# Kernel optimization log

Hardware: AMD Instinct MI355X
Metric: run time of the kernel (lower is better)

Reference implementation:

```python
import jax, jax.numpy as jnp
import numpy as np

NUM_EMBEDDINGS = 1024
EMBEDDING_DIM = 64


def setup_inputs() -> dict:
    key = jax.random.key(0)
    k1, k2 = jax.random.split(key)
    x = jax.random.normal(k1, (32, 64, 32, 32), dtype=jnp.float32)
    # embeddings initialized uniform(-1/K, 1/K) as in the torch module
    codebook = jax.random.uniform(
        k2, (NUM_EMBEDDINGS, EMBEDDING_DIM), dtype=jnp.float32,
        minval=-1.0 / NUM_EMBEDDINGS, maxval=1.0 / NUM_EMBEDDINGS)
    return {"x": x, "codebook": codebook}


def reference(x, codebook):
    # x: [B, D, H, W] -> [B, H, W, D]
    xp = jnp.transpose(x, (0, 2, 3, 1))
    B, H, W, D = xp.shape
    K = codebook.shape[0]
    xf = xp.reshape(-1, D)  # [N, D]
    # squared L2 distances via expansion (argmin identical to torch.norm argmin)
    x2 = jnp.sum(xf * xf, axis=1, keepdims=True)          # [N, 1]
    c2 = jnp.sum(codebook * codebook, axis=1)             # [K]
    d2 = x2 - 2.0 * (xf @ codebook.T) + c2[None, :]       # [N, K]
    idx = jnp.argmin(d2, axis=1)                          # [N]
    encodings = jax.nn.one_hot(idx, K, dtype=jnp.float32)  # [N, K]
    quantized = codebook[idx]                             # [N, D] == encodings @ codebook
    quantized = quantized.reshape(B, H, W, D).transpose(0, 3, 1, 2)
    return encodings, quantized
```

## Files before the change

kernel.cpp:

```cpp
#include <hip/hip_runtime.h>

#define N_PIX   32768
#define DIM     64
#define K_CODES 1024
#define NCHUNK  8
#define CHUNK   (K_CODES / NCHUNK)


__global__ __launch_bounds__(256) void c2_kernel(const float* __restrict__ cb,
                                                 float* __restrict__ c2) {
    int k = blockIdx.x * 256 + threadIdx.x;
    if (k >= K_CODES) return;
    const float* row = cb + k * DIM;
    float a0 = 0.f, a1 = 0.f, a2 = 0.f, a3 = 0.f;
#pragma unroll
    for (int d = 0; d < DIM; d += 4) {
        a0 = fmaf(row[d + 0], row[d + 0], a0);
        a1 = fmaf(row[d + 1], row[d + 1], a1);
        a2 = fmaf(row[d + 2], row[d + 2], a2);
        a3 = fmaf(row[d + 3], row[d + 3], a3);
    }
    c2[k] = (a0 + a1) + (a2 + a3);
}

__global__ __launch_bounds__(256, 4) void argmin_lds(const float* __restrict__ x,
                                                     const float* __restrict__ cb,
                                                     const float* __restrict__ c2,
                                                     float2* __restrict__ part) {
    __shared__ alignas(16) float lds_cb[CHUNK][DIM];
    __shared__ float lds_c2[CHUNK];

    int blk    = blockIdx.x;
    int pixblk = blk >> 3;
    int chunk  = blk & 7;
    int t  = threadIdx.x;
    int k0 = chunk * CHUNK;

    {
        const float4* cb4  = reinterpret_cast<const float4*>(cb) + (size_t)k0 * (DIM / 4);
        float4*       lds4 = reinterpret_cast<float4*>(&lds_cb[0][0]);
#pragma unroll
        for (int i = 0; i < (CHUNK * DIM / 4) / 256; ++i)
            lds4[t + i * 256] = cb4[t + i * 256];
        if (t < CHUNK) lds_c2[t] = c2[k0 + t];
    }

    int p  = pixblk * 256 + t;
    int bb = p >> 10;
    int hw = p & 1023;

    const float* xbase = x + (size_t)bb * (DIM * 1024) + hw;
    float xv[DIM];
#pragma unroll
    for (int d = 0; d < DIM; ++d) xv[d] = xbase[(size_t)d << 10];

    float s0 = 0.f, s1 = 0.f, s2 = 0.f, s3 = 0.f;
#pragma unroll
    for (int d = 0; d < DIM; d += 4) {
        s0 = fmaf(xv[d + 0], xv[d + 0], s0);
        s1 = fmaf(xv[d + 1], xv[d + 1], s1);
        s2 = fmaf(xv[d + 2], xv[d + 2], s2);
        s3 = fmaf(xv[d + 3], xv[d + 3], s3);
    }
    float x2 = (s0 + s1) + (s2 + s3);

    __syncthreads();

    float best = 1e30f;
    int   bidx = 0;
#pragma unroll 2
    for (int kk = 0; kk < CHUNK; ++kk) {
        const float* crow = &lds_cb[kk][0];
        float c2k = lds_c2[kk];
        float a0 = 0.f, a1 = 0.f, a2 = 0.f, a3 = 0.f;
#pragma unroll
        for (int d = 0; d < DIM; d += 4) {
            float4 w = *reinterpret_cast<const float4*>(crow + d);
            a0 = fmaf(xv[d + 0], w.x, a0);
            a1 = fmaf(xv[d + 1], w.y, a1);
            a2 = fmaf(xv[d + 2], w.z, a2);
            a3 = fmaf(xv[d + 3], w.w, a3);
        }
        float dot = (a0 + a1) + (a2 + a3);
        float u    = x2 - 2.0f * dot;
        float dist = u + c2k;
        int   k    = k0 + kk;
        if (dist < best) { best = dist; bidx = k; }
    }
    float2 r;
    r.x = best;
    r.y = __int_as_float(bidx);
    part[(size_t)chunk * N_PIX + p] = r;
}

__global__ __launch_bounds__(128) void reduce_quant(const float* __restrict__ cb,
                                                    const float2* __restrict__ part,
                                                    int* __restrict__ idx,
                                                    float* __restrict__ quant) {
    int n = blockIdx.x * 128 + threadIdx.x;
    float best = 1e30f;
    int   bi = 0;
#pragma unroll
    for (int c = 0; c < NCHUNK; ++c) {
        float2 r = part[(size_t)c * N_PIX + n];
        if (r.x < best) { best = r.x; bi = __float_as_int(r.y); }
    }
    idx[n] = bi;

    int bb = n >> 10;
    int hw = n & 1023;
    const float4* crow = reinterpret_cast<const float4*>(cb + (size_t)bi * DIM);
    float* qb = quant + (size_t)bb * (DIM * 1024) + hw;
#pragma unroll
    for (int dq = 0; dq < 16; ++dq) {
        float4 cv = crow[dq];
        qb[(size_t)(dq * 4 + 0) << 10] = cv.x;
        qb[(size_t)(dq * 4 + 1) << 10] = cv.y;
        qb[(size_t)(dq * 4 + 2) << 10] = cv.z;
        qb[(size_t)(dq * 4 + 3) << 10] = cv.w;
    }
}

__global__ __launch_bounds__(256) void enc_write(const int* __restrict__ idx,
                                                 float* __restrict__ enc) {
    const int TOT = (N_PIX / 4) * K_CODES;
    int tid = blockIdx.x * 256 + threadIdx.x;
    float4* enc4 = reinterpret_cast<float4*>(enc);
    for (int e = tid; e < TOT; e += 2048 * 256) {
        int n  = e >> 8;
        int j0 = (e & 255) << 2;
        int ir = idx[n];
        float4 v;
        v.x = (ir == j0 + 0) ? 1.0f : 0.0f;
        v.y = (ir == j0 + 1) ? 1.0f : 0.0f;
        v.z = (ir == j0 + 2) ? 1.0f : 0.0f;
        v.w = (ir == j0 + 3) ? 1.0f : 0.0f;
        enc4[e] = v;
    }
}

extern "C" void kernel_launch(void* const* d_in, const int* in_sizes, int n_in,
                              void* d_out, int out_size, void* d_ws, size_t ws_size,
                              hipStream_t stream) {
    const float* x  = (const float*)d_in[0];
    const float* cb = (const float*)d_in[1];

    float*  c2   = (float*)d_ws;
    float2* part = (float2*)((char*)d_ws + 4096);
    int*    idx  = (int*)((char*)d_ws + 4096 + (size_t)NCHUNK * N_PIX * 8);

    float* enc   = (float*)d_out;
    float* quant = (float*)d_out + (size_t)N_PIX * K_CODES;

    c2_kernel<<<K_CODES / 256, 256, 0, stream>>>(cb, c2);
    argmin_lds<<<(N_PIX / 256) * NCHUNK, 256, 0, stream>>>(x, cb, c2, part);
    reduce_quant<<<N_PIX / 128, 128, 0, stream>>>(cb, part, idx, quant);
    enc_write<<<2048, 256, 0, stream>>>(idx, enc);
}
```

Baseline: 255.0 us.

## Replace per-pixel argmin with register-tiled GEMM-style kernel fused with quantize

Replaces the per-thread dot-product argmin, which held 64 x values per thread and split the codebook into 8 chunks with a separate partial reduction, with a 128-pixel by 1024-code register-tiled kernel. Each thread computes an 8x8 outer-product tile from LDS-staged transposed x and codebook slices, prefetching the next codebook chunk into registers while computing. The argmin is reduced in-block via shuffles and LDS, and the quantized gather/write is fused in, removing the partial buffer and the reduce kernel. It raises register and LDS pressure and adds index tie-breaking that the previous code did not have.

```diff
diff --git a/kernel.cpp b/kernel.cpp
--- a/kernel.cpp
+++ b/kernel.cpp
@@ -1,10 +1,12 @@
 #include <hip/hip_runtime.h>
 
-#define N_PIX   32768
-#define DIM     64
-#define K_CODES 1024
-#define NCHUNK  8
-#define CHUNK   (K_CODES / NCHUNK)
+#define N_PIX    32768
+#define DIM      64
+#define K_CODES  1024
+#define NCHUNK   4
+#define CHUNK    256
+#define BPIX     128
+#define CS_STR   260
 
 
 __global__ __launch_bounds__(256) void c2_kernel(const float* __restrict__ cb,
@@ -23,101 +25,169 @@
     c2[k] = (a0 + a1) + (a2 + a3);
 }
 
-__global__ __launch_bounds__(256, 4) void argmin_lds(const float* __restrict__ x,
-                                                     const float* __restrict__ cb,
-                                                     const float* __restrict__ c2,
-                                                     float2* __restrict__ part) {
-    __shared__ alignas(16) float lds_cb[CHUNK][DIM];
-    __shared__ float lds_c2[CHUNK];
-
-    int blk    = blockIdx.x;
-    int pixblk = blk >> 3;
-    int chunk  = blk & 7;
-    int t  = threadIdx.x;
-    int k0 = chunk * CHUNK;
-
-    {
-        const float4* cb4  = reinterpret_cast<const float4*>(cb) + (size_t)k0 * (DIM / 4);
-        float4*       lds4 = reinterpret_cast<float4*>(&lds_cb[0][0]);
-#pragma unroll
-        for (int i = 0; i < (CHUNK * DIM / 4) / 256; ++i)
-            lds4[t + i * 256] = cb4[t + i * 256];
-        if (t < CHUNK) lds_c2[t] = c2[k0 + t];
-    }
-
-    int p  = pixblk * 256 + t;
-    int bb = p >> 10;
-    int hw = p & 1023;
-
-    const float* xbase = x + (size_t)bb * (DIM * 1024) + hw;
-    float xv[DIM];
-#pragma unroll
-    for (int d = 0; d < DIM; ++d) xv[d] = xbase[(size_t)d << 10];
-
-    float s0 = 0.f, s1 = 0.f, s2 = 0.f, s3 = 0.f;
-#pragma unroll
-    for (int d = 0; d < DIM; d += 4) {
-        s0 = fmaf(xv[d + 0], xv[d + 0], s0);
-        s1 = fmaf(xv[d + 1], xv[d + 1], s1);
-        s2 = fmaf(xv[d + 2], xv[d + 2], s2);
-        s3 = fmaf(xv[d + 3], xv[d + 3], s3);
-    }
-    float x2 = (s0 + s1) + (s2 + s3);
-
+__global__ __launch_bounds__(512, 2) void argmin_tile(const float* __restrict__ x,
+                                                      const float* __restrict__ cb,
+                                                      const float* __restrict__ c2,
+                                                      int* __restrict__ idx,
+                                                      float* __restrict__ quant) {
+    __shared__ alignas(16) float xs[DIM * BPIX];
+    __shared__ alignas(16) float cs[DIM * CS_STR];
+    __shared__ float  xn[BPIX];
+    __shared__ float2 red[4][BPIX];
+
+    const int t      = threadIdx.x;
+    const int blk    = blockIdx.x;
+    const int p_base = blk * BPIX;
+    const int bb     = p_base >> 10;
+    const int hw0    = p_base & 1023;
+
+    const float4* x4  = reinterpret_cast<const float4*>(x);
+    const float4* cb4 = reinterpret_cast<const float4*>(cb);
+
+#pragma unroll
+    for (int i = 0; i < 4; ++i) {
+        int fidx = i * 512 + t;
+        int d = fidx >> 5, p4 = fidx & 31;
+        float4 v = x4[(size_t)bb * 16384 + (size_t)d * 256 + (hw0 >> 2) + p4];
+        *reinterpret_cast<float4*>(&xs[d * BPIX + p4 * 4]) = v;
+    }
     __syncthreads();
 
-    float best = 1e30f;
-    int   bidx = 0;
-#pragma unroll 2
-    for (int kk = 0; kk < CHUNK; ++kk) {
-        const float* crow = &lds_cb[kk][0];
-        float c2k = lds_c2[kk];
-        float a0 = 0.f, a1 = 0.f, a2 = 0.f, a3 = 0.f;
+    if (t < BPIX) {
+        float s0 = 0.f, s1 = 0.f, s2 = 0.f, s3 = 0.f;
 #pragma unroll
         for (int d = 0; d < DIM; d += 4) {
-            float4 w = *reinterpret_cast<const float4*>(crow + d);
-            a0 = fmaf(xv[d + 0], w.x, a0);
-            a1 = fmaf(xv[d + 1], w.y, a1);
-            a2 = fmaf(xv[d + 2], w.z, a2);
-            a3 = fmaf(xv[d + 3], w.w, a3);
-        }
-        float dot = (a0 + a1) + (a2 + a3);
-        float u    = x2 - 2.0f * dot;
-        float dist = u + c2k;
-        int   k    = k0 + kk;
-        if (dist < best) { best = dist; bidx = k; }
-    }
-    float2 r;
-    r.x = best;
-    r.y = __int_as_float(bidx);
-    part[(size_t)chunk * N_PIX + p] = r;
-}
-
-__global__ __launch_bounds__(128) void reduce_quant(const float* __restrict__ cb,
-                                                    const float2* __restrict__ part,
-                                                    int* __restrict__ idx,
-                                                    float* __restrict__ quant) {
-    int n = blockIdx.x * 128 + threadIdx.x;
-    float best = 1e30f;
-    int   bi = 0;
-#pragma unroll
+            float v0 = xs[(d + 0) * BPIX + t];
+            float v1 = xs[(d + 1) * BPIX + t];
+            float v2 = xs[(d + 2) * BPIX + t];
+            float v3 = xs[(d + 3) * BPIX + t];
+            s0 = fmaf(v0, v0, s0);
+            s1 = fmaf(v1, v1, s1);
+            s2 = fmaf(v2, v2, s2);
+            s3 = fmaf(v3, v3, s3);
+        }
+        xn[t] = (s0 + s1) + (s2 + s3);
+    }
+
+    const int lane = t & 63, w = t >> 6;
+    const int wy = lane >> 3, wx = lane & 7;
+    const int wr = w >> 2,    wc = w & 3;
+    const int pl0 = wr * 64 + wy * 8;
+    const int kl0 = wc * 64 + wx * 8;
+
+    float bv[8]; int bk[8]; float xnr[8];
+#pragma unroll
+    for (int i = 0; i < 8; ++i) { bv[i] = 1e30f; bk[i] = 0; }
+
+    float4 creg[8];
+#pragma unroll
+    for (int i = 0; i < 8; ++i) {
+        int fidx = i * 512 + t; int k = fidx & 255, dq = fidx >> 8;
+        creg[i] = cb4[(size_t)k * 16 + dq];
+    }
+    __syncthreads();
+
+#pragma unroll
+    for (int i = 0; i < 8; ++i) xnr[i] = xn[pl0 + i];
+
     for (int c = 0; c < NCHUNK; ++c) {
-        float2 r = part[(size_t)c * N_PIX + n];
-        if (r.x < best) { best = r.x; bi = __float_as_int(r.y); }
-    }
-    idx[n] = bi;
-
-    int bb = n >> 10;
-    int hw = n & 1023;
-    const float4* crow = reinterpret_cast<const float4*>(cb + (size_t)bi * DIM);
-    float* qb = quant + (size_t)bb * (DIM * 1024) + hw;
-#pragma unroll
-    for (int dq = 0; dq < 16; ++dq) {
-        float4 cv = crow[dq];
-        qb[(size_t)(dq * 4 + 0) << 10] = cv.x;
-        qb[(size_t)(dq * 4 + 1) << 10] = cv.y;
-        qb[(size_t)(dq * 4 + 2) << 10] = cv.z;
-        qb[(size_t)(dq * 4 + 3) << 10] = cv.w;
+#pragma unroll
+        for (int i = 0; i < 8; ++i) {
+            int fidx = i * 512 + t; int k = fidx & 255, dq = fidx >> 8;
+            cs[(4 * dq + 0) * CS_STR + k] = creg[i].x;
+            cs[(4 * dq + 1) * CS_STR + k] = creg[i].y;
+            cs[(4 * dq + 2) * CS_STR + k] = creg[i].z;
+            cs[(4 * dq + 3) * CS_STR + k] = creg[i].w;
+        }
+        if (c + 1 < NCHUNK) {
+#pragma unroll
+            for (int i = 0; i < 8; ++i) {
+                int fidx = i * 512 + t; int k = fidx & 255, dq = fidx >> 8;
+                creg[i] = cb4[(size_t)((c + 1) * CHUNK + k) * 16 + dq];
+            }
+        }
+        __syncthreads();
+
+        float acc[8][8];
+#pragma unroll
+        for (int i = 0; i < 8; ++i)
+#pragma unroll
+            for (int j = 0; j < 8; ++j) acc[i][j] = 0.f;
+
+#pragma unroll 4
+        for (int d = 0; d < DIM; ++d) {
+            const float* xr = &xs[d * BPIX + pl0];
+            const float* cr = &cs[d * CS_STR + kl0];
+            float4 xlo = *reinterpret_cast<const float4*>(xr);
+            float4 xhi = *reinterpret_cast<const float4*>(xr + 4);
+            float4 clo = *reinterpret_cast<const float4*>(cr);
+            float4 chi = *reinterpret_cast<const float4*>(cr + 4);
+#define ROW(i, xi) \
+            acc[i][0] = fmaf(xi, clo.x, acc[i][0]); \
+            acc[i][1] = fmaf(xi, clo.y, acc[i][1]); \
+            acc[i][2] = fmaf(xi, clo.z, acc[i][2]); \
+            acc[i][3] = fmaf(xi, clo.w, acc[i][3]); \
+            acc[i][4] = fmaf(xi, chi.x, acc[i][4]); \
+            acc[i][5] = fmaf(xi, chi.y, acc[i][5]); \
+            acc[i][6] = fmaf(xi, chi.z, acc[i][6]); \
+            acc[i][7] = fmaf(xi, chi.w, acc[i][7]);
+            ROW(0, xlo.x) ROW(1, xlo.y) ROW(2, xlo.z) ROW(3, xlo.w)
+            ROW(4, xhi.x) ROW(5, xhi.y) ROW(6, xhi.z) ROW(7, xhi.w)
+#undef ROW
+        }
+
+        float4 c2lo = *reinterpret_cast<const float4*>(&c2[c * CHUNK + kl0]);
+        float4 c2hi = *reinterpret_cast<const float4*>(&c2[c * CHUNK + kl0 + 4]);
+        float c2a[8] = {c2lo.x, c2lo.y, c2lo.z, c2lo.w, c2hi.x, c2hi.y, c2hi.z, c2hi.w};
+#pragma unroll
+        for (int i = 0; i < 8; ++i) {
+#pragma unroll
+            for (int j = 0; j < 8; ++j) {
+                int   k    = c * CHUNK + kl0 + j;
+                float u    = xnr[i] - 2.0f * acc[i][j];
+                float dist = u + c2a[j];
+                if (dist < bv[i]) { bv[i] = dist; bk[i] = k; }
+            }
+        }
+        __syncthreads();
+    }
+
+#pragma unroll
+    for (int i = 0; i < 8; ++i) {
+#pragma unroll
+        for (int off = 1; off <= 4; off <<= 1) {
+            float ov = __shfl_xor(bv[i], off);
+            int   ok = __shfl_xor(bk[i], off);
+            if (ov < bv[i] || (ov == bv[i] && ok < bk[i])) { bv[i] = ov; bk[i] = ok; }
+        }
+    }
+    if (wx == 0) {
+#pragma unroll
+        for (int i = 0; i < 8; ++i)
+            red[wc][pl0 + i] = make_float2(bv[i], __int_as_float(bk[i]));
+    }
+    __syncthreads();
+
+    if (t < BPIX) {
+        float fv = 1e30f; int fk = 0;
+#pragma unroll
+        for (int cc = 0; cc < 4; ++cc) {
+            float2 r  = red[cc][t];
+            int    rk = __float_as_int(r.y);
+            if (r.x < fv || (r.x == fv && rk < fk)) { fv = r.x; fk = rk; }
+        }
+        idx[p_base + t] = fk;
+
+        const float4* crow = cb4 + (size_t)fk * 16;
+        float* qb = quant + (size_t)bb * (DIM * 1024) + (hw0 + t);
+#pragma unroll
+        for (int dq = 0; dq < 16; ++dq) {
+            float4 cv = crow[dq];
+            qb[(size_t)(dq * 4 + 0) << 10] = cv.x;
+            qb[(size_t)(dq * 4 + 1) << 10] = cv.y;
+            qb[(size_t)(dq * 4 + 2) << 10] = cv.z;
+            qb[(size_t)(dq * 4 + 3) << 10] = cv.w;
+        }
     }
 }
 
@@ -145,15 +215,13 @@
     const float* x  = (const float*)d_in[0];
     const float* cb = (const float*)d_in[1];
 
-    float*  c2   = (float*)d_ws;
-    float2* part = (float2*)((char*)d_ws + 4096);
-    int*    idx  = (int*)((char*)d_ws + 4096 + (size_t)NCHUNK * N_PIX * 8);
+    float* c2  = (float*)d_ws;
+    int*   idx = (int*)((char*)d_ws + 4096);
 
     float* enc   = (float*)d_out;
     float* quant = (float*)d_out + (size_t)N_PIX * K_CODES;
 
     c2_kernel<<<K_CODES / 256, 256, 0, stream>>>(cb, c2);
-    argmin_lds<<<(N_PIX / 256) * NCHUNK, 256, 0, stream>>>(x, cb, c2, part);
-    reduce_quant<<<N_PIX / 128, 128, 0, stream>>>(cb, part, idx, quant);
+    argmin_tile<<<N_PIX / BPIX, 512, 0, stream>>>(x, cb, c2, idx, quant);
     enc_write<<<2048, 256, 0, stream>>>(idx, enc);
 }
```

Result: faster. 208.9 us (-18.1%).
